# Optimization experiments

Measured on AMD Instinct MI355X. Metric: run time of the kernel, lower is better.

## Reference

```python
import jax, jax.numpy as jnp
import numpy as np

N = 50000          # num_nodes
E = 1600000        # num directed edges
IN_C = 128         # in_channels
OUT_C = 128        # out_channels
HEADS = 8
HFD = OUT_C // HEADS  # head_feat_dim = 16
NEG_SLOPE = 0.2


def setup_inputs() -> dict:
    key = jax.random.key(0)
    k1, k2, k3, k4, k5 = jax.random.split(key, 5)
    node_feats = jax.random.normal(k1, (N, IN_C), dtype=jnp.float32)
    edge_index = jax.random.randint(k2, (2, E), 0, N, dtype=jnp.int64)
    # parameters (xavier-ish scale, kept small so exp() stays in range)
    W = jax.random.normal(k3, (OUT_C, IN_C), dtype=jnp.float32) * (1.0 / np.sqrt(IN_C))
    a_left = jax.random.normal(k4, (HFD, HEADS), dtype=jnp.float32) * 0.1
    a_right = jax.random.normal(k5, (HFD, HEADS), dtype=jnp.float32) * 0.1
    bias = jnp.zeros((OUT_C,), dtype=jnp.float32)
    return {"node_feats": node_feats, "edge_index": edge_index,
            "W": W, "a_left": a_left, "a_right": a_right, "bias": bias}


def reference(node_feats, edge_index, W, a_left, a_right, bias):
    n = node_feats.shape[0]
    # embedding: Linear without bias, then split into heads -> [n, h, c]
    emb = (node_feats @ W.T).reshape(n, HEADS, HFD)
    # per-node attention logit halves: sum_c emb[n,h,c] * a[c,h] -> [n, h]
    left = jnp.einsum('nhc,ch->nh', emb, a_left)
    right = jnp.einsum('nhc,ch->nh', emb, a_right)
    src = edge_index[0]
    dst = edge_index[1]
    # edge logit: score(src, dst) uses a_left on src, a_right on dst
    e = left[src] + right[dst]                       # [E, h]
    e = jnp.where(e >= 0, e, NEG_SLOPE * e)          # leaky relu(0.2)
    w = jnp.exp(e)                                   # [E, h] (module uses raw exp)
    denom = jax.ops.segment_sum(w, dst, num_segments=n)  # [n, h]
    attn = w / denom[dst]                            # [E, h]
    msg = emb[src] * attn[:, :, None]                # [E, h, c]
    out = jax.ops.segment_sum(msg, dst, num_segments=n)  # [n, h, c]
    # concat heads + bias
    out = out.reshape(n, HEADS * HFD) + bias
    return out
```

## Files before the change

### kernel.cpp

```cpp
#include <hip/hip_runtime.h>
#include <hip/hip_bf16.h>

#define N_NODES 50000
#define N_EDGES 1600000
#define HEADS 8
#define HFD 16
#define CH 128

#define PART 128
#define NB 391
#define BCAP 5120
#define PA_T 512
#define PA_CHUNK 6400
#define PA_PER 13
#define PA_BLOCKS 250

typedef __bf16 bf16x8 __attribute__((ext_vector_type(8)));
typedef __bf16 bf16x4 __attribute__((ext_vector_type(4)));
typedef float f32x4 __attribute__((ext_vector_type(4)));

__device__ __forceinline__ float bf_lo(unsigned u) { return __uint_as_float(u << 16); }
__device__ __forceinline__ float bf_hi(unsigned u) { return __uint_as_float(u & 0xffff0000u); }

__global__ __launch_bounds__(256) void k_splitw(const float* __restrict__ x,
                                                __bf16* __restrict__ hi,
                                                __bf16* __restrict__ lo,
                                                int n4) {
  int t = blockIdx.x * 256 + threadIdx.x;
  if (t >= n4) return;
  f32x4 v = ((const f32x4*)x)[t];
  bf16x4 h, l;
#pragma unroll
  for (int i = 0; i < 4; ++i) {
    __bf16 hb = (__bf16)v[i];
    h[i] = hb;
    l[i] = (__bf16)(v[i] - (float)hb);
  }
  ((bf16x4*)hi)[t] = h;
  ((bf16x4*)lo)[t] = l;
}

__global__ __launch_bounds__(64) void k_emb(const float* __restrict__ X,
                                            const __bf16* __restrict__ Whi,
                                            const __bf16* __restrict__ Wlo,
                                            const float* __restrict__ aL,
                                            const float* __restrict__ aR,
                                            __bf16* __restrict__ embb,
                                            float* __restrict__ leftp,
                                            float* __restrict__ rightp) {
  int ntile = blockIdx.x;
  int lane = threadIdx.x;
  int c = lane & 15, quad = lane >> 4;
  const float* xp = X + (size_t)(ntile * 16 + c) * CH + quad * 8;
  bf16x8 xh[4], xl[4];
#pragma unroll
  for (int ks = 0; ks < 4; ++ks) {
    float4 x0 = *(const float4*)(xp + ks * 32);
    float4 x1 = *(const float4*)(xp + ks * 32 + 4);
    float xv[8] = {x0.x, x0.y, x0.z, x0.w, x1.x, x1.y, x1.z, x1.w};
#pragma unroll
    for (int j = 0; j < 8; ++j) {
      __bf16 hb = (__bf16)xv[j];
      xh[ks][j] = hb;
      xl[ks][j] = (__bf16)(xv[j] - (float)hb);
    }
  }
#pragma unroll
  for (int h = 0; h < HEADS; ++h) {
    const __bf16* wp = Whi + (size_t)(h * 16 + c) * CH + quad * 8;
    const __bf16* wlp = Wlo + (size_t)(h * 16 + c) * CH + quad * 8;
    f32x4 acc = {0.f, 0.f, 0.f, 0.f};
#pragma unroll
    for (int ks = 0; ks < 4; ++ks) {
      bf16x8 wh = *(const bf16x8*)(wp + ks * 32);
      bf16x8 wl = *(const bf16x8*)(wlp + ks * 32);
      acc = __builtin_amdgcn_mfma_f32_16x16x32_bf16(xl[ks], wh, acc, 0, 0, 0);
      acc = __builtin_amdgcn_mfma_f32_16x16x32_bf16(xh[ks], wl, acc, 0, 0, 0);
      acc = __builtin_amdgcn_mfma_f32_16x16x32_bf16(xh[ks], wh, acc, 0, 0, 0);
    }
    float aLv = aL[c * HEADS + h];
    float aRv = aR[c * HEADS + h];
#pragma unroll
    for (int r = 0; r < 4; ++r) {
      int node = ntile * 16 + quad * 4 + r;
      float v = acc[r];
      embb[(size_t)node * CH + h * HFD + c] = (__bf16)v;
      float sl = v * aLv, sr = v * aRv;
#pragma unroll
      for (int mm = 1; mm < 16; mm <<= 1) {
        sl += __shfl_xor(sl, mm);
        sr += __shfl_xor(sr, mm);
      }
      if (c == 0) {
        leftp[node * HEADS + h] = sl;
        rightp[node * HEADS + h] = sr;
      }
    }
  }
}

__global__ __launch_bounds__(PA_T) void k_bucket(const int* __restrict__ ei,
                                                 int* __restrict__ bucket_cnt,
                                                 unsigned* __restrict__ ebuf) {
  __shared__ unsigned sp[PA_CHUNK];
  __shared__ int hist[NB];
  __shared__ int lcur[NB];
  __shared__ int wbase[NB];
  __shared__ int scn[PA_T];
  int t = threadIdx.x;
  int base = blockIdx.x * PA_CHUNK;
  for (int i = t; i < NB; i += PA_T) hist[i] = 0;
  __syncthreads();
  unsigned pk[PA_PER];
#pragma unroll
  for (int i = 0; i < PA_PER; ++i) {
    int e = t + i * PA_T;
    pk[i] = 0xffffffffu;
    if (e < PA_CHUNK) {
      int src = ei[base + e];
      int dst = ei[N_EDGES + base + e];
      pk[i] = ((unsigned)(dst >> 7) << 23) | ((unsigned)(dst & 127) << 16) |
              (unsigned)src;
      atomicAdd(&hist[dst >> 7], 1);
    }
  }
  __syncthreads();
  scn[t] = (t < NB) ? hist[t] : 0;
  __syncthreads();
  int val = scn[t];
  for (int d = 1; d < PA_T; d <<= 1) {
    int o = (t >= d) ? scn[t - d] : 0;
    __syncthreads();
    val += o;
    scn[t] = val;
    __syncthreads();
  }
  if (t < NB) {
    int hv = hist[t];
    int lstart = val - hv;
    lcur[t] = lstart;
    int prior = hv ? atomicAdd(&bucket_cnt[t], hv) : 0;
    wbase[t] = t * BCAP + prior - lstart;
  }
  __syncthreads();
#pragma unroll
  for (int i = 0; i < PA_PER; ++i) {
    if (pk[i] != 0xffffffffu) {
      int b = pk[i] >> 23;
      int pos = atomicAdd(&lcur[b], 1);
      sp[pos] = pk[i];
    }
  }
  __syncthreads();
  for (int i = t; i < PA_CHUNK; i += PA_T) {
    unsigned p = sp[i];
    int b = p >> 23;
    int slot = wbase[b] + i;
    if (slot < (b + 1) * BCAP) ebuf[slot] = p;
  }
}

__global__ __launch_bounds__(512) void k_csr(const int* __restrict__ bucket_cnt,
                                             const unsigned* __restrict__ ebuf,
                                             int* __restrict__ rowptr,
                                             int* __restrict__ deg,
                                             unsigned short* __restrict__ csr) {
  __shared__ int hist[PART];
  __shared__ int pfx[PART];
  __shared__ int cur[PART];
  int b = blockIdx.x, t = threadIdx.x;
  int cnt = bucket_cnt[b];
  if (cnt > BCAP) cnt = BCAP;
  int ebase = b * BCAP;
  if (t < PART) hist[t] = 0;
  __syncthreads();
  for (int e = t; e < cnt; e += 512)
    atomicAdd(&hist[(ebuf[ebase + e] >> 16) & 127], 1);
  __syncthreads();
  if (t < PART) pfx[t] = hist[t];
  __syncthreads();
  for (int d = 1; d < PART; d <<= 1) {
    int v = 0;
    if (t < PART) { v = pfx[t]; if (t >= d) v += pfx[t - d]; }
    __syncthreads();
    if (t < PART) pfx[t] = v;
    __syncthreads();
  }
  if (t < PART) {
    int excl = pfx[t] - hist[t];
    cur[t] = ebase + excl;
    int dst = b * PART + t;
    if (dst < N_NODES) {
      rowptr[dst] = ebase + excl;
      deg[dst] = hist[t];
    }
  }
  __syncthreads();
  for (int e = t; e < cnt; e += 512) {
    unsigned p = ebuf[ebase + e];
    int pos = atomicAdd(&cur[(p >> 16) & 127], 1);
    csr[pos] = (unsigned short)(p & 0xffffu);
  }
}

__global__ __launch_bounds__(256) void k_aggr(const int* __restrict__ rowptr,
                                              const int* __restrict__ deg,
                                              const unsigned short* __restrict__ csr,
                                              const __bf16* __restrict__ embb,
                                              const float* __restrict__ leftp,
                                              const float* __restrict__ rightp,
                                              const float* __restrict__ bias,
                                              float* __restrict__ out) {
  int dst = blockIdx.x * 4 + (threadIdx.x >> 6);
  int lane = threadIdx.x & 63;
  int g = lane >> 4;
  int m = lane & 15;
  int h = m >> 1;
  int beg = __builtin_amdgcn_readfirstlane(rowptr[dst]);
  int cnt = __builtin_amdgcn_readfirstlane(deg[dst]);
  float r = rightp[dst * HEADS + h];
  float acc[8] = {0.f, 0.f, 0.f, 0.f, 0.f, 0.f, 0.f, 0.f};
  float dsum = 0.f;
  for (int e0 = 0; e0 < cnt; e0 += 8) {
    int i0 = e0 + g, i1 = e0 + 4 + g;
    bool a0 = i0 < cnt, a1 = i1 < cnt;
    int s0 = csr[beg + (a0 ? i0 : 0)];
    int s1 = csr[beg + (a1 ? i1 : 0)];
    uint4 u0 = ((const uint4*)(embb + (size_t)s0 * CH))[m];
    uint4 u1 = ((const uint4*)(embb + (size_t)s1 * CH))[m];
    float l0 = leftp[s0 * HEADS + h];
    float l1 = leftp[s1 * HEADS + h];
    float x0 = l0 + r;
    x0 = (x0 >= 0.f) ? x0 : 0.2f * x0;
    float w0 = a0 ? __expf(x0) : 0.f;
    float x1 = l1 + r;
    x1 = (x1 >= 0.f) ? x1 : 0.2f * x1;
    float w1 = a1 ? __expf(x1) : 0.f;
    dsum += w0 + w1;
    acc[0] += w0 * bf_lo(u0.x) + w1 * bf_lo(u1.x);
    acc[1] += w0 * bf_hi(u0.x) + w1 * bf_hi(u1.x);
    acc[2] += w0 * bf_lo(u0.y) + w1 * bf_lo(u1.y);
    acc[3] += w0 * bf_hi(u0.y) + w1 * bf_hi(u1.y);
    acc[4] += w0 * bf_lo(u0.z) + w1 * bf_lo(u1.z);
    acc[5] += w0 * bf_hi(u0.z) + w1 * bf_hi(u1.z);
    acc[6] += w0 * bf_lo(u0.w) + w1 * bf_lo(u1.w);
    acc[7] += w0 * bf_hi(u0.w) + w1 * bf_hi(u1.w);
  }
#pragma unroll
  for (int mask = 16; mask <= 32; mask <<= 1) {
    dsum += __shfl_xor(dsum, mask);
#pragma unroll
    for (int j = 0; j < 8; ++j) acc[j] += __shfl_xor(acc[j], mask);
  }
  if (g == 0) {
    float inv = (dsum > 0.f) ? 1.0f / dsum : 0.f;
    float4 b0 = ((const float4*)bias)[2 * m];
    float4 b1 = ((const float4*)bias)[2 * m + 1];
    float4 o0 = {acc[0] * inv + b0.x, acc[1] * inv + b0.y,
                 acc[2] * inv + b0.z, acc[3] * inv + b0.w};
    float4 o1 = {acc[4] * inv + b1.x, acc[5] * inv + b1.y,
                 acc[6] * inv + b1.z, acc[7] * inv + b1.w};
    ((float4*)(out + (size_t)dst * CH))[2 * m] = o0;
    ((float4*)(out + (size_t)dst * CH))[2 * m + 1] = o1;
  }
}

extern "C" void kernel_launch(void* const* d_in, const int* in_sizes, int n_in,
                              void* d_out, int out_size, void* d_ws, size_t ws_size,
                              hipStream_t stream) {
  const float* X = (const float*)d_in[0];
  const int* ei = (const int*)d_in[1];
  const float* W = (const float*)d_in[2];
  const float* al = (const float*)d_in[3];
  const float* ar = (const float*)d_in[4];
  const float* bias = (const float*)d_in[5];
  float* out = (float*)d_out;

  unsigned* ebuf = (unsigned*)d_ws;
  unsigned short* csr = (unsigned short*)(ebuf + (size_t)NB * BCAP);
  int* rowptr = (int*)(csr + (size_t)NB * BCAP);
  int* deg = rowptr + N_NODES;
  int* bucket_cnt = deg + N_NODES;
  float* leftp = (float*)(bucket_cnt + 400);
  float* rightp = leftp + (size_t)N_NODES * HEADS;
  __bf16* embb = (__bf16*)(rightp + (size_t)N_NODES * HEADS);
  __bf16* Whi = embb + (size_t)N_NODES * CH;
  __bf16* Wlo = Whi + CH * CH;

  hipMemsetAsync(bucket_cnt, 0, NB * sizeof(int), stream);

  k_splitw<<<(CH * CH / 4 + 255) / 256, 256, 0, stream>>>(W, Whi, Wlo, CH * CH / 4);
  k_emb<<<N_NODES / 16, 64, 0, stream>>>(X, Whi, Wlo, al, ar, embb, leftp, rightp);
  k_bucket<<<PA_BLOCKS, PA_T, 0, stream>>>(ei, bucket_cnt, ebuf);
  k_csr<<<NB, 512, 0, stream>>>(bucket_cnt, ebuf, rowptr, deg, csr);
  k_aggr<<<N_NODES / 4, 256, 0, stream>>>(rowptr, deg, csr, embb, leftp, rightp, bias, out);
}
```

Measured before the change: 234.7 us.

## Fuse CSR build into aggregation kernel and fold memset into weight split

Drops the separate CSR kernel. Each aggregation block now loads its destination bucket into shared memory, builds the per-destination histogram, prefix sum and local CSR there, then aggregates 64 destinations per block, with two blocks splitting each bucket. The bucket-count memset moves into the weight-split kernel, and the bucketing kernel gets smaller chunks across more blocks and is launched before the embedding kernel. This saves a launch and the global round trip of the CSR arrays. In exchange, each bucket is sorted twice (once per half-block), the large shared-memory footprint lowers occupancy, and fewer but longer blocks may load-balance worse.

```diff
diff --git a/kernel.cpp b/kernel.cpp
--- a/kernel.cpp
+++ b/kernel.cpp
@@ -11,9 +11,9 @@
 #define NB 391
 #define BCAP 5120
 #define PA_T 512
-#define PA_CHUNK 6400
-#define PA_PER 13
-#define PA_BLOCKS 250
+#define PA_CHUNK 3200
+#define PA_PER 7
+#define PA_BLOCKS 500
 
 typedef __bf16 bf16x8 __attribute__((ext_vector_type(8)));
 typedef __bf16 bf16x4 __attribute__((ext_vector_type(4)));
@@ -25,8 +25,10 @@
 __global__ __launch_bounds__(256) void k_splitw(const float* __restrict__ x,
                                                 __bf16* __restrict__ hi,
                                                 __bf16* __restrict__ lo,
-                                                int n4) {
+                                                int n4,
+                                                int* __restrict__ bucket_cnt) {
   int t = blockIdx.x * 256 + threadIdx.x;
+  if (t < NB) bucket_cnt[t] = 0;
   if (t >= n4) return;
   f32x4 v = ((const f32x4*)x)[t];
   bf16x4 h, l;
@@ -160,108 +162,111 @@
   }
 }
 
-__global__ __launch_bounds__(512) void k_csr(const int* __restrict__ bucket_cnt,
-                                             const unsigned* __restrict__ ebuf,
-                                             int* __restrict__ rowptr,
-                                             int* __restrict__ deg,
-                                             unsigned short* __restrict__ csr) {
-  __shared__ int hist[PART];
-  __shared__ int pfx[PART];
-  __shared__ int cur[PART];
-  int b = blockIdx.x, t = threadIdx.x;
-  int cnt = bucket_cnt[b];
-  if (cnt > BCAP) cnt = BCAP;
-  int ebase = b * BCAP;
-  if (t < PART) hist[t] = 0;
-  __syncthreads();
-  for (int e = t; e < cnt; e += 512)
-    atomicAdd(&hist[(ebuf[ebase + e] >> 16) & 127], 1);
-  __syncthreads();
-  if (t < PART) pfx[t] = hist[t];
-  __syncthreads();
-  for (int d = 1; d < PART; d <<= 1) {
-    int v = 0;
-    if (t < PART) { v = pfx[t]; if (t >= d) v += pfx[t - d]; }
-    __syncthreads();
-    if (t < PART) pfx[t] = v;
-    __syncthreads();
-  }
-  if (t < PART) {
-    int excl = pfx[t] - hist[t];
-    cur[t] = ebase + excl;
-    int dst = b * PART + t;
-    if (dst < N_NODES) {
-      rowptr[dst] = ebase + excl;
-      deg[dst] = hist[t];
-    }
-  }
-  __syncthreads();
-  for (int e = t; e < cnt; e += 512) {
-    unsigned p = ebuf[ebase + e];
-    int pos = atomicAdd(&cur[(p >> 16) & 127], 1);
-    csr[pos] = (unsigned short)(p & 0xffffu);
-  }
-}
-
-__global__ __launch_bounds__(256) void k_aggr(const int* __restrict__ rowptr,
-                                              const int* __restrict__ deg,
-                                              const unsigned short* __restrict__ csr,
+__global__ __launch_bounds__(512) void k_aggr(const int* __restrict__ bucket_cnt,
+                                              const unsigned* __restrict__ ebuf,
                                               const __bf16* __restrict__ embb,
                                               const float* __restrict__ leftp,
                                               const float* __restrict__ rightp,
                                               const float* __restrict__ bias,
                                               float* __restrict__ out) {
-  int dst = blockIdx.x * 4 + (threadIdx.x >> 6);
-  int lane = threadIdx.x & 63;
+  __shared__ unsigned sp[BCAP];
+  __shared__ unsigned short su[BCAP];
+  __shared__ int hist[PART];
+  __shared__ int pfx[PART];
+  __shared__ int cur[PART];
+  int b = blockIdx.x >> 1;
+  int half = blockIdx.x & 1;
+  int t = threadIdx.x;
+  int cnt = bucket_cnt[b];
+  if (cnt > BCAP) cnt = BCAP;
+  int ebase = b * BCAP;
+  if (t < PART) hist[t] = 0;
+  __syncthreads();
+  for (int e = t; e < cnt; e += 512) {
+    unsigned p = ebuf[ebase + e];
+    sp[e] = p;
+    atomicAdd(&hist[(p >> 16) & 127], 1);
+  }
+  __syncthreads();
+  if (t < PART) pfx[t] = hist[t];
+  __syncthreads();
+  for (int d = 1; d < PART; d <<= 1) {
+    int v = 0;
+    if (t < PART) { v = pfx[t]; if (t >= d) v += pfx[t - d]; }
+    __syncthreads();
+    if (t < PART) pfx[t] = v;
+    __syncthreads();
+  }
+  if (t < PART) {
+    int excl = pfx[t] - hist[t];
+    pfx[t] = excl;
+    cur[t] = excl;
+  }
+  __syncthreads();
+  for (int e = t; e < cnt; e += 512) {
+    unsigned p = sp[e];
+    int pos = atomicAdd(&cur[(p >> 16) & 127], 1);
+    su[pos] = (unsigned short)(p & 0xffffu);
+  }
+  __syncthreads();
+
+  int wv = t >> 6;
+  int lane = t & 63;
   int g = lane >> 4;
   int m = lane & 15;
   int h = m >> 1;
-  int beg = __builtin_amdgcn_readfirstlane(rowptr[dst]);
-  int cnt = __builtin_amdgcn_readfirstlane(deg[dst]);
-  float r = rightp[dst * HEADS + h];
-  float acc[8] = {0.f, 0.f, 0.f, 0.f, 0.f, 0.f, 0.f, 0.f};
-  float dsum = 0.f;
-  for (int e0 = 0; e0 < cnt; e0 += 8) {
-    int i0 = e0 + g, i1 = e0 + 4 + g;
-    bool a0 = i0 < cnt, a1 = i1 < cnt;
-    int s0 = csr[beg + (a0 ? i0 : 0)];
-    int s1 = csr[beg + (a1 ? i1 : 0)];
-    uint4 u0 = ((const uint4*)(embb + (size_t)s0 * CH))[m];
-    uint4 u1 = ((const uint4*)(embb + (size_t)s1 * CH))[m];
-    float l0 = leftp[s0 * HEADS + h];
-    float l1 = leftp[s1 * HEADS + h];
-    float x0 = l0 + r;
-    x0 = (x0 >= 0.f) ? x0 : 0.2f * x0;
-    float w0 = a0 ? __expf(x0) : 0.f;
-    float x1 = l1 + r;
-    x1 = (x1 >= 0.f) ? x1 : 0.2f * x1;
-    float w1 = a1 ? __expf(x1) : 0.f;
-    dsum += w0 + w1;
-    acc[0] += w0 * bf_lo(u0.x) + w1 * bf_lo(u1.x);
-    acc[1] += w0 * bf_hi(u0.x) + w1 * bf_hi(u1.x);
-    acc[2] += w0 * bf_lo(u0.y) + w1 * bf_lo(u1.y);
-    acc[3] += w0 * bf_hi(u0.y) + w1 * bf_hi(u1.y);
-    acc[4] += w0 * bf_lo(u0.z) + w1 * bf_lo(u1.z);
-    acc[5] += w0 * bf_hi(u0.z) + w1 * bf_hi(u1.z);
-    acc[6] += w0 * bf_lo(u0.w) + w1 * bf_lo(u1.w);
-    acc[7] += w0 * bf_hi(u0.w) + w1 * bf_hi(u1.w);
-  }
-#pragma unroll
-  for (int mask = 16; mask <= 32; mask <<= 1) {
-    dsum += __shfl_xor(dsum, mask);
-#pragma unroll
-    for (int j = 0; j < 8; ++j) acc[j] += __shfl_xor(acc[j], mask);
-  }
-  if (g == 0) {
-    float inv = (dsum > 0.f) ? 1.0f / dsum : 0.f;
-    float4 b0 = ((const float4*)bias)[2 * m];
-    float4 b1 = ((const float4*)bias)[2 * m + 1];
-    float4 o0 = {acc[0] * inv + b0.x, acc[1] * inv + b0.y,
-                 acc[2] * inv + b0.z, acc[3] * inv + b0.w};
-    float4 o1 = {acc[4] * inv + b1.x, acc[5] * inv + b1.y,
-                 acc[6] * inv + b1.z, acc[7] * inv + b1.w};
-    ((float4*)(out + (size_t)dst * CH))[2 * m] = o0;
-    ((float4*)(out + (size_t)dst * CH))[2 * m + 1] = o1;
+#pragma unroll
+  for (int k = 0; k < 8; ++k) {
+    int dl = half * 64 + wv * 8 + k;
+    int dst = b * PART + dl;
+    bool valid = dst < N_NODES;
+    int beg = pfx[dl];
+    int cd = hist[dl];
+    float r = valid ? rightp[dst * HEADS + h] : 0.f;
+    float acc[8] = {0.f, 0.f, 0.f, 0.f, 0.f, 0.f, 0.f, 0.f};
+    float dsum = 0.f;
+    for (int e0 = 0; e0 < cd; e0 += 8) {
+      int i0 = e0 + g, i1 = e0 + 4 + g;
+      bool a0 = i0 < cd, a1 = i1 < cd;
+      int s0 = su[beg + (a0 ? i0 : 0)];
+      int s1 = su[beg + (a1 ? i1 : 0)];
+      uint4 u0 = ((const uint4*)(embb + (size_t)s0 * CH))[m];
+      uint4 u1 = ((const uint4*)(embb + (size_t)s1 * CH))[m];
+      float l0 = leftp[s0 * HEADS + h];
+      float l1 = leftp[s1 * HEADS + h];
+      float x0 = l0 + r;
+      x0 = (x0 >= 0.f) ? x0 : 0.2f * x0;
+      float w0 = a0 ? __expf(x0) : 0.f;
+      float x1 = l1 + r;
+      x1 = (x1 >= 0.f) ? x1 : 0.2f * x1;
+      float w1 = a1 ? __expf(x1) : 0.f;
+      dsum += w0 + w1;
+      acc[0] += w0 * bf_lo(u0.x) + w1 * bf_lo(u1.x);
+      acc[1] += w0 * bf_hi(u0.x) + w1 * bf_hi(u1.x);
+      acc[2] += w0 * bf_lo(u0.y) + w1 * bf_lo(u1.y);
+      acc[3] += w0 * bf_hi(u0.y) + w1 * bf_hi(u1.y);
+      acc[4] += w0 * bf_lo(u0.z) + w1 * bf_lo(u1.z);
+      acc[5] += w0 * bf_hi(u0.z) + w1 * bf_hi(u1.z);
+      acc[6] += w0 * bf_lo(u0.w) + w1 * bf_lo(u1.w);
+      acc[7] += w0 * bf_hi(u0.w) + w1 * bf_hi(u1.w);
+    }
+#pragma unroll
+    for (int mask = 16; mask <= 32; mask <<= 1) {
+      dsum += __shfl_xor(dsum, mask);
+#pragma unroll
+      for (int j = 0; j < 8; ++j) acc[j] += __shfl_xor(acc[j], mask);
+    }
+    if (g == 0 && valid) {
+      float inv = (dsum > 0.f) ? 1.0f / dsum : 0.f;
+      float4 b0 = ((const float4*)bias)[2 * m];
+      float4 b1 = ((const float4*)bias)[2 * m + 1];
+      float4 o0 = {acc[0] * inv + b0.x, acc[1] * inv + b0.y,
+                   acc[2] * inv + b0.z, acc[3] * inv + b0.w};
+      float4 o1 = {acc[4] * inv + b1.x, acc[5] * inv + b1.y,
+                   acc[6] * inv + b1.z, acc[7] * inv + b1.w};
+      ((float4*)(out + (size_t)dst * CH))[2 * m] = o0;
+      ((float4*)(out + (size_t)dst * CH))[2 * m + 1] = o1;
+    }
   }
 }
 
@@ -277,21 +282,16 @@
   float* out = (float*)d_out;
 
   unsigned* ebuf = (unsigned*)d_ws;
-  unsigned short* csr = (unsigned short*)(ebuf + (size_t)NB * BCAP);
-  int* rowptr = (int*)(csr + (size_t)NB * BCAP);
-  int* deg = rowptr + N_NODES;
-  int* bucket_cnt = deg + N_NODES;
-  float* leftp = (float*)(bucket_cnt + 400);
-  float* rightp = leftp + (size_t)N_NODES * HEADS;
-  __bf16* embb = (__bf16*)(rightp + (size_t)N_NODES * HEADS);
+  __bf16* embb = (__bf16*)(ebuf + (size_t)NB * BCAP);
   __bf16* Whi = embb + (size_t)N_NODES * CH;
   __bf16* Wlo = Whi + CH * CH;
-
-  hipMemsetAsync(bucket_cnt, 0, NB * sizeof(int), stream);
-
-  k_splitw<<<(CH * CH / 4 + 255) / 256, 256, 0, stream>>>(W, Whi, Wlo, CH * CH / 4);
+  float* leftp = (float*)(Wlo + CH * CH);
+  float* rightp = leftp + (size_t)N_NODES * HEADS;
+  int* bucket_cnt = (int*)(rightp + (size_t)N_NODES * HEADS);
+
+  k_splitw<<<(CH * CH / 4 + 255) / 256, 256, 0, stream>>>(W, Whi, Wlo, CH * CH / 4,
+                                                          bucket_cnt);
+  k_bucket<<<PA_BLOCKS, PA_T, 0, stream>>>(ei, bucket_cnt, ebuf);
   k_emb<<<N_NODES / 16, 64, 0, stream>>>(X, Whi, Wlo, al, ar, embb, leftp, rightp);
-  k_bucket<<<PA_BLOCKS, PA_T, 0, stream>>>(ei, bucket_cnt, ebuf);
-  k_csr<<<NB, 512, 0, stream>>>(bucket_cnt, ebuf, rowptr, deg, csr);
-  k_aggr<<<N_NODES / 4, 256, 0, stream>>>(rowptr, deg, csr, embb, leftp, rightp, bias, out);
-}
+  k_aggr<<<NB * 2, 512, 0, stream>>>(bucket_cnt, ebuf, embb, leftp, rightp, bias, out);
+}
```

Result: faster. 215.0 us (-8.4%).
